# Performance work log

Measured on AMD Instinct MI355X. Metric: run time of the kernel, lower is better.

The kernel has to match this reference:

```python
import math
import jax, jax.numpy as jnp
import numpy as np

H = 1024        # hidden_size
NH = 16         # num_attention_heads
HD = H // NH    # attention_head_size
I = 4096        # intermediate_size
B, S = 4, 2048
LN_EPS = 1e-5


def setup_inputs() -> dict:
    key = jax.random.key(0)
    ks = jax.random.split(key, 12)
    s = 0.02
    return {
        "x": jax.random.normal(ks[0], (B, S, H), dtype=jnp.float32),
        "ln1_g": jnp.ones((H,), jnp.float32),
        "ln1_b": jnp.zeros((H,), jnp.float32),
        "qkv_w": jax.random.normal(ks[1], (H, 3 * H), jnp.float32) * s,
        "qkv_b": jnp.zeros((3 * H,), jnp.float32),
        "out_w": jax.random.normal(ks[2], (H, H), jnp.float32) * s,
        "out_b": jnp.zeros((H,), jnp.float32),
        "ln2_g": jnp.ones((H,), jnp.float32),
        "ln2_b": jnp.zeros((H,), jnp.float32),
        "w1": jax.random.normal(ks[3], (H, I), jnp.float32) * s,
        "b1": jnp.zeros((I,), jnp.float32),
        "w2": jax.random.normal(ks[4], (I, H), jnp.float32) * s,
        "b2": jnp.zeros((H,), jnp.float32),
    }


def _layernorm(x, g, b):
    mu = jnp.mean(x, axis=-1, keepdims=True)
    var = jnp.mean(jnp.square(x - mu), axis=-1, keepdims=True)
    return (x - mu) * jax.lax.rsqrt(var + LN_EPS) * g + b


def _gelu_tanh(x):
    c = math.sqrt(2.0 / math.pi)
    return 0.5 * x * (1.0 + jnp.tanh(c * (x + 0.044715 * x * x * x)))


def reference(x, ln1_g, ln1_b, qkv_w, qkv_b, out_w, out_b, ln2_g, ln2_b, w1, b1, w2, b2):
    b, s, _ = x.shape
    h = _layernorm(x, ln1_g, ln1_b)
    qkv = h @ qkv_w + qkv_b                      # [B,S,3H]
    q, k, v = jnp.split(qkv, 3, axis=-1)
    # [B,S,H] -> [B,NH,S,HD]
    def heads(t):
        return t.reshape(b, s, NH, HD).transpose(0, 2, 1, 3)
    q, k, v = heads(q), heads(k), heads(v)
    scores = jnp.einsum("bhqd,bhkd->bhqk", q, k) / math.sqrt(HD)
    probs = jax.nn.softmax(scores, axis=-1)
    attn = jnp.einsum("bhqk,bhkd->bhqd", probs, v)
    attn = attn.transpose(0, 2, 1, 3).reshape(b, s, H)
    attn = attn @ out_w + out_b
    x = x + attn
    h2 = _layernorm(x, ln2_g, ln2_b)
    mlp = _gelu_tanh(h2 @ w1 + b1) @ w2 + b2
    x = x + mlp
    return x
```

## Files before the change

### kernel.cpp

```cpp
#include <hip/hip_runtime.h>
#include <math.h>

#define H 1024
#define NHEAD 16
#define HDIM 64
#define IDIM 4096
#define BATCH 4
#define SEQ 2048
#define NTOK 8192
#define LN_EPS 1e-5f

typedef __bf16 bf16x8 __attribute__((ext_vector_type(8)));
typedef __bf16 bf16x4 __attribute__((ext_vector_type(4)));
typedef float f32x4 __attribute__((ext_vector_type(4)));
typedef unsigned short ushort8 __attribute__((ext_vector_type(8)));
typedef unsigned short ushort4v __attribute__((ext_vector_type(4)));

__device__ __forceinline__ unsigned short f2bf(float f) {
  union { float f; unsigned int u; } v; v.f = f;
  unsigned int u = v.u;
  return (unsigned short)((u + 0x7FFFu + ((u >> 16) & 1u)) >> 16);
}

__global__ void transpose_cast_kernel(const float* __restrict__ W,
                                      unsigned short* __restrict__ Wt,
                                      int K, int N) {
  __shared__ unsigned short tile[32][33];
  int n0 = blockIdx.x * 32, k0 = blockIdx.y * 32;
  int tx = threadIdx.x, ty = threadIdx.y;
#pragma unroll
  for (int i = 0; i < 4; i++) {
    int k = ty + i * 8;
    tile[tx][k] = f2bf(W[(size_t)(k0 + k) * N + n0 + tx]);
  }
  __syncthreads();
#pragma unroll
  for (int i = 0; i < 4; i++) {
    int n = ty + i * 8;
    Wt[(size_t)(n0 + n) * K + k0 + tx] = tile[n][tx];
  }
}

__global__ void transpose_v_kernel(const unsigned short* __restrict__ qkv,
                                   unsigned short* __restrict__ vt) {
  __shared__ unsigned short tile[32][33];
  int s0 = blockIdx.x * 32, d0 = blockIdx.y * 32;
  int bh = blockIdx.z, b = bh >> 4, h = bh & 15;
  int tx = threadIdx.x, ty = threadIdx.y;
#pragma unroll
  for (int i = 0; i < 4; i++) {
    int s = ty + i * 8;
    tile[s][tx] = qkv[((size_t)b * SEQ + s0 + s) * (3 * H) + 2 * H + h * HDIM + d0 + tx];
  }
  __syncthreads();
#pragma unroll
  for (int i = 0; i < 4; i++) {
    int d = ty + i * 8;
    vt[((size_t)bh * HDIM + d0 + d) * SEQ + s0 + tx] = tile[tx][d];
  }
}

__global__ __launch_bounds__(256)
void layernorm_kernel(const float* __restrict__ x, const float* __restrict__ g,
                      const float* __restrict__ b, unsigned short* __restrict__ out) {
  __shared__ float sb[4];
  int row = blockIdx.x;
  int tid = threadIdx.x;
  const float4* xr = (const float4*)(x + (size_t)row * H);
  float4 v = xr[tid];
  float s = v.x + v.y + v.z + v.w;
#pragma unroll
  for (int o = 32; o > 0; o >>= 1) s += __shfl_down(s, o);
  if ((tid & 63) == 0) sb[tid >> 6] = s;
  __syncthreads();
  float mu = (sb[0] + sb[1] + sb[2] + sb[3]) * (1.0f / H);
  __syncthreads();
  float dx = v.x - mu, dy = v.y - mu, dz = v.z - mu, dw = v.w - mu;
  float s2 = dx * dx + dy * dy + dz * dz + dw * dw;
#pragma unroll
  for (int o = 32; o > 0; o >>= 1) s2 += __shfl_down(s2, o);
  if ((tid & 63) == 0) sb[tid >> 6] = s2;
  __syncthreads();
  float var = (sb[0] + sb[1] + sb[2] + sb[3]) * (1.0f / H);
  float rs = rsqrtf(var + LN_EPS);
  float4 gv = ((const float4*)g)[tid];
  float4 bv = ((const float4*)b)[tid];
  ushort4v ov;
  ov[0] = f2bf(dx * rs * gv.x + bv.x);
  ov[1] = f2bf(dy * rs * gv.y + bv.y);
  ov[2] = f2bf(dz * rs * gv.z + bv.z);
  ov[3] = f2bf(dw * rs * gv.w + bv.w);
  ((ushort4v*)(out + (size_t)row * H))[tid] = ov;
}

template <int EPI>
__global__ __launch_bounds__(256)
void gemm_bt_kernel(const unsigned short* __restrict__ A,
                    const unsigned short* __restrict__ Bt,
                    const float* __restrict__ bias,
                    const float* __restrict__ res,
                    void* __restrict__ out, int M, int N, int K) {
  __shared__ __align__(16) unsigned short As[128 * 32];
  __shared__ __align__(16) unsigned short Bs[128 * 32];
  int tid = threadIdx.x;
  int wave = tid >> 6, lane = tid & 63;
  int quad = lane >> 4, l16 = lane & 15;
  int wm = wave >> 1, wn = wave & 1;
  int m0 = blockIdx.y * 128, n0 = blockIdx.x * 128;
  f32x4 acc[4][4];
#pragma unroll
  for (int i = 0; i < 4; i++)
#pragma unroll
    for (int j = 0; j < 4; j++) acc[i][j] = (f32x4){0.f, 0.f, 0.f, 0.f};

  int rl = (lane >> 2);
  int cphys = lane & 3;
  for (int k0 = 0; k0 < K; k0 += 32) {
    __syncthreads();
#pragma unroll
    for (int t = 0; t < 2; t++) {
      int ch = wave * 2 + t;
      int rloc = ch * 16 + rl;
      int clog = cphys ^ ((rloc >> 1) & 3);
      const unsigned short* ga = A + (size_t)(m0 + rloc) * K + k0 + clog * 8;
      __builtin_amdgcn_global_load_lds(
          (const __attribute__((address_space(1))) unsigned int*)ga,
          (__attribute__((address_space(3))) unsigned int*)(As + ch * 512), 16, 0, 0);
      const unsigned short* gb = Bt + (size_t)(n0 + rloc) * K + k0 + clog * 8;
      __builtin_amdgcn_global_load_lds(
          (const __attribute__((address_space(1))) unsigned int*)gb,
          (__attribute__((address_space(3))) unsigned int*)(Bs + ch * 512), 16, 0, 0);
    }
    __syncthreads();
    bf16x8 af[4], bfv[4];
#pragma unroll
    for (int i = 0; i < 4; i++) {
      int ra = wm * 64 + i * 16 + l16;
      af[i] = *(const bf16x8*)&As[ra * 32 + ((quad ^ ((ra >> 1) & 3)) << 3)];
      int rb = wn * 64 + i * 16 + l16;
      bfv[i] = *(const bf16x8*)&Bs[rb * 32 + ((quad ^ ((rb >> 1) & 3)) << 3)];
    }
#pragma unroll
    for (int i = 0; i < 4; i++)
#pragma unroll
      for (int j = 0; j < 4; j++)
        acc[i][j] = __builtin_amdgcn_mfma_f32_16x16x32_bf16(af[i], bfv[j], acc[i][j], 0, 0, 0);
  }
#pragma unroll
  for (int i = 0; i < 4; i++) {
#pragma unroll
    for (int j = 0; j < 4; j++) {
      int col = n0 + wn * 64 + j * 16 + l16;
      float bc = bias[col];
#pragma unroll
      for (int r = 0; r < 4; r++) {
        int row = m0 + wm * 64 + i * 16 + quad * 4 + r;
        float v = acc[i][j][r] + bc;
        size_t off = (size_t)row * N + col;
        if (EPI == 0) {
          ((unsigned short*)out)[off] = f2bf(v);
        } else if (EPI == 1) {
          float t = 0.7978845608028654f * (v + 0.044715f * v * v * v);
          float gl = 0.5f * v * (1.0f + tanhf(t));
          ((unsigned short*)out)[off] = f2bf(gl);
        } else {
          ((float*)out)[off] = v + res[off];
        }
      }
    }
  }
}

__global__ __launch_bounds__(256)
void flash_attn_kernel(const unsigned short* __restrict__ qkv,
                       const unsigned short* __restrict__ vt,
                       unsigned short* __restrict__ attn_out) {
  constexpr int LPs = 72;
  __shared__ __align__(16) unsigned short Ks[64 * 64];
  __shared__ __align__(16) unsigned short Ps[4 * 64 * LPs];
  int tid = threadIdx.x;
  int wave = tid >> 6, lane = tid & 63;
  int quad = lane >> 4, l16 = lane & 15;
  int bh = blockIdx.y, b = bh >> 4, h = bh & 15;
  int qblk = blockIdx.x * 256 + wave * 64;
  const size_t qrow = 3 * H;
  const size_t tok0 = (size_t)b * SEQ;
  const size_t vbase = (size_t)bh * HDIM * SEQ;
  unsigned short* Psw = Ps + wave * 64 * LPs;

  bf16x8 qb[4][2];
#pragma unroll
  for (int mb = 0; mb < 4; mb++)
#pragma unroll
    for (int ks = 0; ks < 2; ks++)
      qb[mb][ks] = *(const bf16x8*)&qkv[(tok0 + qblk + mb * 16 + l16) * qrow +
                                        h * HDIM + ks * 32 + quad * 8];

  float l_part[4] = {0.f, 0.f, 0.f, 0.f};
  f32x4 o_acc[4][4];
#pragma unroll
  for (int mb = 0; mb < 4; mb++)
#pragma unroll
    for (int db = 0; db < 4; db++) o_acc[mb][db] = (f32x4){0.f, 0.f, 0.f, 0.f};

  int srow = lane >> 3;
  int schunk = (lane & 7) ^ srow;

  for (int kv0 = 0; kv0 < SEQ; kv0 += 64) {
    __syncthreads();
#pragma unroll
    for (int t = 0; t < 2; t++) {
      int rbase = wave * 16 + t * 8;
      const unsigned short* ga =
          &qkv[(tok0 + kv0 + rbase + srow) * qrow + H + h * HDIM + schunk * 8];
      __builtin_amdgcn_global_load_lds(
          (const __attribute__((address_space(1))) unsigned int*)ga,
          (__attribute__((address_space(3))) unsigned int*)(Ks + rbase * 64), 16, 0, 0);
    }
    bf16x8 va[4][2];
#pragma unroll
    for (int db = 0; db < 4; db++)
#pragma unroll
      for (int ks = 0; ks < 2; ks++)
        va[db][ks] = *(const bf16x8*)&vt[vbase + (size_t)(db * 16 + l16) * SEQ +
                                         kv0 + ks * 32 + quad * 8];
    __syncthreads();
#pragma unroll
    for (int nb = 0; nb < 4; nb++) {
      int row = nb * 16 + l16;
      bf16x8 ka[2];
#pragma unroll
      for (int ks = 0; ks < 2; ks++) {
        int pc = (ks * 4 + quad) ^ (row & 7);
        ka[ks] = *(const bf16x8*)&Ks[row * 64 + pc * 8];
      }
      f32x4 st[4];
#pragma unroll
      for (int mb = 0; mb < 4; mb++) st[mb] = (f32x4){0.f, 0.f, 0.f, 0.f};
#pragma unroll
      for (int ks = 0; ks < 2; ks++)
#pragma unroll
        for (int mb = 0; mb < 4; mb++)
          st[mb] = __builtin_amdgcn_mfma_f32_16x16x32_bf16(ka[ks], qb[mb][ks], st[mb], 0, 0, 0);
#pragma unroll
      for (int mb = 0; mb < 4; mb++) {
        float p0 = __expf(st[mb][0] * 0.125f);
        float p1 = __expf(st[mb][1] * 0.125f);
        float p2 = __expf(st[mb][2] * 0.125f);
        float p3 = __expf(st[mb][3] * 0.125f);
        l_part[mb] += (p0 + p1) + (p2 + p3);
        bf16x4 pk = {(__bf16)p0, (__bf16)p1, (__bf16)p2, (__bf16)p3};
        *(bf16x4*)&Psw[(mb * 16 + l16) * LPs + nb * 16 + quad * 4] = pk;
      }
    }
    __asm__ volatile("s_waitcnt lgkmcnt(0)" ::: "memory");
#pragma unroll
    for (int ks = 0; ks < 2; ks++) {
      bf16x8 pb[4];
#pragma unroll
      for (int mb = 0; mb < 4; mb++)
        pb[mb] = *(const bf16x8*)&Psw[(mb * 16 + l16) * LPs + ks * 32 + quad * 8];
#pragma unroll
      for (int db = 0; db < 4; db++)
#pragma unroll
        for (int mb = 0; mb < 4; mb++)
          o_acc[mb][db] = __builtin_amdgcn_mfma_f32_16x16x32_bf16(va[db][ks], pb[mb],
                                                                  o_acc[mb][db], 0, 0, 0);
    }
  }
#pragma unroll
  for (int mb = 0; mb < 4; mb++) {
    l_part[mb] += __shfl_xor(l_part[mb], 16);
    l_part[mb] += __shfl_xor(l_part[mb], 32);
    l_part[mb] = 1.0f / l_part[mb];
  }
#pragma unroll
  for (int mb = 0; mb < 4; mb++) {
#pragma unroll
    for (int db = 0; db < 4; db++) {
      ushort4v o;
#pragma unroll
      for (int r = 0; r < 4; r++) o[r] = f2bf(o_acc[mb][db][r] * l_part[mb]);
      *(ushort4v*)&attn_out[(tok0 + qblk + mb * 16 + l16) * H + h * HDIM +
                            db * 16 + quad * 4] = o;
    }
  }
}

extern "C" void kernel_launch(void* const* d_in, const int* in_sizes, int n_in,
                              void* d_out, int out_size, void* d_ws, size_t ws_size,
                              hipStream_t stream) {
  const float* x = (const float*)d_in[0];
  const float* ln1_g = (const float*)d_in[1];
  const float* ln1_b = (const float*)d_in[2];
  const float* qkv_w = (const float*)d_in[3];
  const float* qkv_b = (const float*)d_in[4];
  const float* out_w = (const float*)d_in[5];
  const float* out_b = (const float*)d_in[6];
  const float* ln2_g = (const float*)d_in[7];
  const float* ln2_b = (const float*)d_in[8];
  const float* w1 = (const float*)d_in[9];
  const float* b1 = (const float*)d_in[10];
  const float* w2 = (const float*)d_in[11];
  const float* b2 = (const float*)d_in[12];
  float* outp = (float*)d_out;

  size_t off = 0;
  auto take = [&](size_t n) {
    char* p = (char*)d_ws + off;
    off += (n + 255) & ~(size_t)255;
    return p;
  };
  unsigned short* h1 = (unsigned short*)take((size_t)NTOK * H * 2);
  unsigned short* qkvb = (unsigned short*)take((size_t)NTOK * 3 * H * 2);
  unsigned short* attn = (unsigned short*)take((size_t)NTOK * H * 2);
  float* x1 = (float*)take((size_t)NTOK * H * 4);
  unsigned short* qkvwt = (unsigned short*)take((size_t)3 * H * H * 2);
  unsigned short* outwt = (unsigned short*)take((size_t)H * H * 2);
  unsigned short* w1t = (unsigned short*)take((size_t)H * IDIM * 2);
  unsigned short* w2t = (unsigned short*)take((size_t)H * IDIM * 2);
  unsigned short* h2 = h1;
  unsigned short* mid = qkvb;
  unsigned short* vt = (unsigned short*)x1;

  dim3 tb(32, 8);
  transpose_cast_kernel<<<dim3(3 * H / 32, H / 32), tb, 0, stream>>>(qkv_w, qkvwt, H, 3 * H);
  transpose_cast_kernel<<<dim3(H / 32, H / 32), tb, 0, stream>>>(out_w, outwt, H, H);
  transpose_cast_kernel<<<dim3(IDIM / 32, H / 32), tb, 0, stream>>>(w1, w1t, H, IDIM);
  transpose_cast_kernel<<<dim3(H / 32, IDIM / 32), tb, 0, stream>>>(w2, w2t, IDIM, H);

  layernorm_kernel<<<NTOK, 256, 0, stream>>>(x, ln1_g, ln1_b, h1);
  gemm_bt_kernel<0><<<dim3(3 * H / 128, NTOK / 128), 256, 0, stream>>>(
      h1, qkvwt, qkv_b, nullptr, qkvb, NTOK, 3 * H, H);
  transpose_v_kernel<<<dim3(SEQ / 32, HDIM / 32, BATCH * NHEAD), tb, 0, stream>>>(qkvb, vt);
  flash_attn_kernel<<<dim3(SEQ / 256, BATCH * NHEAD), 256, 0, stream>>>(qkvb, vt, attn);
  gemm_bt_kernel<2><<<dim3(H / 128, NTOK / 128), 256, 0, stream>>>(
      attn, outwt, out_b, x, x1, NTOK, H, H);
  layernorm_kernel<<<NTOK, 256, 0, stream>>>(x1, ln2_g, ln2_b, h2);
  gemm_bt_kernel<1><<<dim3(IDIM / 128, NTOK / 128), 256, 0, stream>>>(
      h2, w1t, b1, nullptr, mid, NTOK, IDIM, H);
  gemm_bt_kernel<2><<<dim3(H / 128, NTOK / 128), 256, 0, stream>>>(
      mid, w2t, b2, x1, outp, NTOK, H, IDIM);
}
```

Baseline: 695.3 us.

## Transpose GEMM MFMA operands for vectorized epilogue and shrink attention query tile

The GEMM swaps the MFMA operand order so each lane holds four consecutive columns. That lets the epilogue load bias and residual as float4 and store packed bf16x4 or float4 instead of scalar strided writes. GELU-tanh is rewritten as an equivalent sigmoid form using __expf in place of tanhf. Flash attention now gives each wave 32 query rows instead of 64, doubling the grid to 1024 blocks and cutting registers and LDS per block. The cost is that K/V tiles are reloaded twice as often per query.

New measurement: 696.4 us. No clear change (+0.1%).

```diff
diff --git a/kernel.cpp b/kernel.cpp
--- a/kernel.cpp
+++ b/kernel.cpp
@@ -144,28 +144,35 @@
     for (int i = 0; i < 4; i++)
 #pragma unroll
       for (int j = 0; j < 4; j++)
-        acc[i][j] = __builtin_amdgcn_mfma_f32_16x16x32_bf16(af[i], bfv[j], acc[i][j], 0, 0, 0);
-  }
-#pragma unroll
-  for (int i = 0; i < 4; i++) {
+        acc[i][j] = __builtin_amdgcn_mfma_f32_16x16x32_bf16(bfv[j], af[i], acc[i][j], 0, 0, 0);
+  }
+#pragma unroll
+  for (int i = 0; i < 4; i++) {
+    int m = m0 + wm * 64 + i * 16 + l16;
 #pragma unroll
     for (int j = 0; j < 4; j++) {
-      int col = n0 + wn * 64 + j * 16 + l16;
-      float bc = bias[col];
-#pragma unroll
-      for (int r = 0; r < 4; r++) {
-        int row = m0 + wm * 64 + i * 16 + quad * 4 + r;
-        float v = acc[i][j][r] + bc;
-        size_t off = (size_t)row * N + col;
-        if (EPI == 0) {
-          ((unsigned short*)out)[off] = f2bf(v);
-        } else if (EPI == 1) {
-          float t = 0.7978845608028654f * (v + 0.044715f * v * v * v);
-          float gl = 0.5f * v * (1.0f + tanhf(t));
-          ((unsigned short*)out)[off] = f2bf(gl);
-        } else {
-          ((float*)out)[off] = v + res[off];
-        }
+      int nb = n0 + wn * 64 + j * 16 + quad * 4;
+      float4 bv4 = *(const float4*)&bias[nb];
+      float v0 = acc[i][j][0] + bv4.x;
+      float v1 = acc[i][j][1] + bv4.y;
+      float v2 = acc[i][j][2] + bv4.z;
+      float v3 = acc[i][j][3] + bv4.w;
+      size_t off = (size_t)m * N + nb;
+      if (EPI == 0) {
+        bf16x4 pk = {(__bf16)v0, (__bf16)v1, (__bf16)v2, (__bf16)v3};
+        *(bf16x4*)&((unsigned short*)out)[off] = pk;
+      } else if (EPI == 1) {
+        float g0 = v0 / (1.f + __expf(-1.5957691216057308f * (v0 + 0.044715f * v0 * v0 * v0)));
+        float g1 = v1 / (1.f + __expf(-1.5957691216057308f * (v1 + 0.044715f * v1 * v1 * v1)));
+        float g2 = v2 / (1.f + __expf(-1.5957691216057308f * (v2 + 0.044715f * v2 * v2 * v2)));
+        float g3 = v3 / (1.f + __expf(-1.5957691216057308f * (v3 + 0.044715f * v3 * v3 * v3)));
+        bf16x4 pk = {(__bf16)g0, (__bf16)g1, (__bf16)g2, (__bf16)g3};
+        *(bf16x4*)&((unsigned short*)out)[off] = pk;
+      } else {
+        float4 rv = *(const float4*)&res[off];
+        float4 o4;
+        o4.x = v0 + rv.x; o4.y = v1 + rv.y; o4.z = v2 + rv.z; o4.w = v3 + rv.w;
+        *(float4*)&((float*)out)[off] = o4;
       }
     }
   }
@@ -177,29 +184,29 @@
                        unsigned short* __restrict__ attn_out) {
   constexpr int LPs = 72;
   __shared__ __align__(16) unsigned short Ks[64 * 64];
-  __shared__ __align__(16) unsigned short Ps[4 * 64 * LPs];
+  __shared__ __align__(16) unsigned short Ps[4 * 32 * LPs];
   int tid = threadIdx.x;
   int wave = tid >> 6, lane = tid & 63;
   int quad = lane >> 4, l16 = lane & 15;
   int bh = blockIdx.y, b = bh >> 4, h = bh & 15;
-  int qblk = blockIdx.x * 256 + wave * 64;
+  int qblk = blockIdx.x * 128 + wave * 32;
   const size_t qrow = 3 * H;
   const size_t tok0 = (size_t)b * SEQ;
   const size_t vbase = (size_t)bh * HDIM * SEQ;
-  unsigned short* Psw = Ps + wave * 64 * LPs;
-
-  bf16x8 qb[4][2];
-#pragma unroll
-  for (int mb = 0; mb < 4; mb++)
+  unsigned short* Psw = Ps + wave * 32 * LPs;
+
+  bf16x8 qb[2][2];
+#pragma unroll
+  for (int mb = 0; mb < 2; mb++)
 #pragma unroll
     for (int ks = 0; ks < 2; ks++)
       qb[mb][ks] = *(const bf16x8*)&qkv[(tok0 + qblk + mb * 16 + l16) * qrow +
                                         h * HDIM + ks * 32 + quad * 8];
 
-  float l_part[4] = {0.f, 0.f, 0.f, 0.f};
-  f32x4 o_acc[4][4];
-#pragma unroll
-  for (int mb = 0; mb < 4; mb++)
+  float l_part[2] = {0.f, 0.f};
+  f32x4 o_acc[2][4];
+#pragma unroll
+  for (int mb = 0; mb < 2; mb++)
 #pragma unroll
     for (int db = 0; db < 4; db++) o_acc[mb][db] = (f32x4){0.f, 0.f, 0.f, 0.f};
 
@@ -234,16 +241,16 @@
         int pc = (ks * 4 + quad) ^ (row & 7);
         ka[ks] = *(const bf16x8*)&Ks[row * 64 + pc * 8];
       }
-      f32x4 st[4];
-#pragma unroll
-      for (int mb = 0; mb < 4; mb++) st[mb] = (f32x4){0.f, 0.f, 0.f, 0.f};
+      f32x4 st[2];
+#pragma unroll
+      for (int mb = 0; mb < 2; mb++) st[mb] = (f32x4){0.f, 0.f, 0.f, 0.f};
 #pragma unroll
       for (int ks = 0; ks < 2; ks++)
 #pragma unroll
-        for (int mb = 0; mb < 4; mb++)
+        for (int mb = 0; mb < 2; mb++)
           st[mb] = __builtin_amdgcn_mfma_f32_16x16x32_bf16(ka[ks], qb[mb][ks], st[mb], 0, 0, 0);
 #pragma unroll
-      for (int mb = 0; mb < 4; mb++) {
+      for (int mb = 0; mb < 2; mb++) {
         float p0 = __expf(st[mb][0] * 0.125f);
         float p1 = __expf(st[mb][1] * 0.125f);
         float p2 = __expf(st[mb][2] * 0.125f);
@@ -256,26 +263,26 @@
     __asm__ volatile("s_waitcnt lgkmcnt(0)" ::: "memory");
 #pragma unroll
     for (int ks = 0; ks < 2; ks++) {
-      bf16x8 pb[4];
-#pragma unroll
-      for (int mb = 0; mb < 4; mb++)
+      bf16x8 pb[2];
+#pragma unroll
+      for (int mb = 0; mb < 2; mb++)
         pb[mb] = *(const bf16x8*)&Psw[(mb * 16 + l16) * LPs + ks * 32 + quad * 8];
 #pragma unroll
       for (int db = 0; db < 4; db++)
 #pragma unroll
-        for (int mb = 0; mb < 4; mb++)
+        for (int mb = 0; mb < 2; mb++)
           o_acc[mb][db] = __builtin_amdgcn_mfma_f32_16x16x32_bf16(va[db][ks], pb[mb],
                                                                   o_acc[mb][db], 0, 0, 0);
     }
   }
 #pragma unroll
-  for (int mb = 0; mb < 4; mb++) {
+  for (int mb = 0; mb < 2; mb++) {
     l_part[mb] += __shfl_xor(l_part[mb], 16);
     l_part[mb] += __shfl_xor(l_part[mb], 32);
     l_part[mb] = 1.0f / l_part[mb];
   }
 #pragma unroll
-  for (int mb = 0; mb < 4; mb++) {
+  for (int mb = 0; mb < 2; mb++) {
 #pragma unroll
     for (int db = 0; db < 4; db++) {
       ushort4v o;
@@ -333,7 +340,7 @@
   gemm_bt_kernel<0><<<dim3(3 * H / 128, NTOK / 128), 256, 0, stream>>>(
       h1, qkvwt, qkv_b, nullptr, qkvb, NTOK, 3 * H, H);
   transpose_v_kernel<<<dim3(SEQ / 32, HDIM / 32, BATCH * NHEAD), tb, 0, stream>>>(qkvb, vt);
-  flash_attn_kernel<<<dim3(SEQ / 256, BATCH * NHEAD), 256, 0, stream>>>(qkvb, vt, attn);
+  flash_attn_kernel<<<dim3(SEQ / 128, BATCH * NHEAD), 256, 0, stream>>>(qkvb, vt, attn);
   gemm_bt_kernel<2><<<dim3(H / 128, NTOK / 128), 256, 0, stream>>>(
       attn, outwt, out_b, x, x1, NTOK, H, H);
   layernorm_kernel<<<NTOK, 256, 0, stream>>>(x1, ln2_g, ln2_b, h2);
```
